# Performance work log

Measured on AMD Instinct MI355X. Metric: run time of the kernel, lower is better.

## Reference

```python
import jax, jax.numpy as jnp
import numpy as np

N_EMBD = 1024
N_HEAD = 16
HEAD_DIM = N_EMBD // N_HEAD


def setup_inputs() -> dict:
    key = jax.random.key(0)
    k1, k2, k3 = jax.random.split(key, 3)
    B, T, C = 2, 2048, N_EMBD
    x = jax.random.normal(k1, (B, T, C), dtype=jnp.float32)
    # torch nn.Linear(n_embd, 3*n_embd): weight [3C, C], bias [3C]
    W = jax.random.normal(k2, (3 * C, C), dtype=jnp.float32) * (1.0 / np.sqrt(C))
    b = jax.random.normal(k3, (3 * C,), dtype=jnp.float32) * 0.01
    return {"x": x, "W": W, "b": b}


def reference(x, W, b):
    B, T, C = x.shape
    H, D = N_HEAD, HEAD_DIM
    qkv = jnp.einsum('btc,oc->bto', x, W) + b          # [B,T,3C]
    q, k, v = jnp.split(qkv, 3, axis=2)
    # [B,H,T,D]
    q = q.reshape(B, T, H, D).transpose(0, 2, 1, 3)
    k = k.reshape(B, T, H, D).transpose(0, 2, 1, 3)
    v = v.reshape(B, T, H, D).transpose(0, 2, 1, 3)
    scale = 1.0 / np.sqrt(D).astype(np.float32)
    scores = jnp.einsum('bhid,bhjd->bhij', q, k) * scale   # [B,H,T,T]
    causal = jnp.tril(jnp.ones((T, T), dtype=bool))
    w = jnp.where(causal, jax.nn.relu(scores), 0.0)        # ReLU, no softmax
    y = jnp.einsum('bhij,bhjd->bhid', w, v)                # [B,H,T,D]
    return y.transpose(0, 2, 1, 3).reshape(B, T, C)
```

## Files before the change

### kernel.cpp

```cpp
#include <hip/hip_runtime.h>

typedef __bf16 bf16;
typedef __bf16 bf16x8 __attribute__((ext_vector_type(8)));
typedef float  f32x4  __attribute__((ext_vector_type(4)));

#define T_SEQ   2048
#define D_HEAD  64
#define NH      16
#define BH      32
#define C_EMB   1024
#define WS_STRIDE (BH * T_SEQ * D_HEAD)
#define XN (4096 * 1024)
#define WN (3072 * 1024)
#define WS_NEEDED ((size_t)(3 * WS_STRIDE + XN + WN) * 2)
#define CVT_GRID 3584

__device__ __forceinline__ bf16x8 cvt8(float4 a, float4 b) {
    bf16x8 r;
    r[0] = (__bf16)a.x; r[1] = (__bf16)a.y; r[2] = (__bf16)a.z; r[3] = (__bf16)a.w;
    r[4] = (__bf16)b.x; r[5] = (__bf16)b.y; r[6] = (__bf16)b.z; r[7] = (__bf16)b.w;
    return r;
}

__device__ __forceinline__ void gl_lds16(const bf16* g, bf16* l) {
    __builtin_amdgcn_global_load_lds(
        (const __attribute__((address_space(1))) unsigned int*)g,
        (__attribute__((address_space(3))) unsigned int*)l,
        16, 0, 0);
}

__device__ __forceinline__ unsigned pack_bf16(float a, float b) {
    union { __bf16 h[2]; unsigned u; } pk;
    pk.h[0] = (__bf16)a; pk.h[1] = (__bf16)b;
    return pk.u;
}

__global__ __launch_bounds__(256) void cvt_bf16(
    const float* __restrict__ x, const float* __restrict__ W,
    bf16* __restrict__ xb, bf16* __restrict__ wb)
{
    const int t = blockIdx.x * 256 + threadIdx.x;
    const float* src; bf16* dst; int base;
    if (t < XN / 8) { src = x; dst = xb; base = t * 8; }
    else           { src = W; dst = wb; base = (t - XN / 8) * 8; }
    float4 a = *(const float4*)(src + base);
    float4 b = *(const float4*)(src + base + 4);
    *(bf16x8*)(dst + base) = cvt8(a, b);
}

#define LDA(d, qi) {                                                          \
    const bf16* abase_ = Sh + (d)*8192 + (qi)*4096 + l15*64;                  \
    _Pragma("unroll")                                                         \
    for (int ii_ = 0; ii_ < 4; ii_++) {                                       \
        _Pragma("unroll")                                                     \
        for (int dk_ = 0; dk_ < 2; dk_++)                                     \
            aF[ii_][dk_] = *(const bf16x8*)(abase_ + ii_*1024                 \
                                            + (((dk_*4 + l4) ^ k7) * 8));     \
    }                                                                         \
}

#define LDB(d) {                                                              \
    const bf16* bbase_ = Sh + 16384 + (d)*12288 + (w*48 + l15)*64;            \
    _Pragma("unroll")                                                         \
    for (int jj_ = 0; jj_ < 3; jj_++) {                                       \
        _Pragma("unroll")                                                     \
        for (int dk_ = 0; dk_ < 2; dk_++)                                     \
            bF[jj_][dk_] = *(const bf16x8*)(bbase_ + jj_*1024                 \
                                            + (((dk_*4 + l4) ^ k7) * 8));     \
    }                                                                         \
}

#define STA(d, qi, s, ko) gl_lds16(                                           \
    aSrc + (size_t)((qi)*64 + (s)*32) * 1024 + (ko),                          \
    Sh + (d)*8192 + (qi)*4096 + (s)*2048 + w*512)

#define STB(d, u, ko) gl_lds16(                                               \
    bSrc + (size_t)((u)*32) * 1024 + (ko),                                    \
    Sh + 16384 + (d)*12288 + (u)*2048 + w*512)

#define MMA2(qi, ja, jb) {                                                    \
    __builtin_amdgcn_s_setprio(1);                                            \
    _Pragma("unroll")                                                         \
    for (int dk_ = 0; dk_ < 2; dk_++) {                                       \
        _Pragma("unroll")                                                     \
        for (int ii_ = 0; ii_ < 4; ii_++) {                                   \
            acc[(qi)*4 + ii_][ja] = __builtin_amdgcn_mfma_f32_16x16x32_bf16(  \
                aF[ii_][dk_], bF[ja][dk_], acc[(qi)*4 + ii_][ja], 0, 0, 0);   \
            acc[(qi)*4 + ii_][jb] = __builtin_amdgcn_mfma_f32_16x16x32_bf16(  \
                aF[ii_][dk_], bF[jb][dk_], acc[(qi)*4 + ii_][jb], 0, 0, 0);   \
        }                                                                     \
    }                                                                         \
    __builtin_amdgcn_s_setprio(0);                                            \
}

#define MMA1(qi, ja) {                                                        \
    __builtin_amdgcn_s_setprio(1);                                            \
    _Pragma("unroll")                                                         \
    for (int dk_ = 0; dk_ < 2; dk_++) {                                       \
        _Pragma("unroll")                                                     \
        for (int ii_ = 0; ii_ < 4; ii_++)                                     \
            acc[(qi)*4 + ii_][ja] = __builtin_amdgcn_mfma_f32_16x16x32_bf16(  \
                aF[ii_][dk_], bF[ja][dk_], acc[(qi)*4 + ii_][ja], 0, 0, 0);   \
    }                                                                         \
    __builtin_amdgcn_s_setprio(0);                                            \
}

#define BAR   __builtin_amdgcn_s_barrier()
#define LGKM0 asm volatile("s_waitcnt lgkmcnt(0)" ::: "memory")

#define HALF(d, sk)                                                           \
                                                                      \
    LDA(d, 0) LDB(d)                                                          \
    BAR; LGKM0;                                                               \
    MMA2(0, 0, 1)                                                             \
    BAR;                                                                      \
                                                \
    STB(d, 0, sk); STB(d, 1, sk); STB(d, 2, sk);                              \
    STB(d, 3, sk); STB(d, 4, sk); STB(d, 5, sk);                              \
    STA(d, 0, 0, sk); STA(d, 0, 1, sk);                                       \
    BAR;                                                                      \
    MMA1(0, 2)                                                                \
    BAR;                                                                      \
                                                                      \
    LDA(d, 1)                                                                 \
    BAR; LGKM0;                                                               \
    MMA2(1, 0, 1)                                                             \
    BAR;                                                                      \
                                                    \
    STA(d, 1, 0, sk); STA(d, 1, 1, sk);                                       \
    BAR;                                                                      \
    MMA1(1, 2)                                                                \
    asm volatile("s_waitcnt vmcnt(10)" ::: "memory");                         \
    BAR;

__global__ __launch_bounds__(256, 2) void qkv_gemm5(
    const bf16* __restrict__ xb, const bf16* __restrict__ wb,
    const float* __restrict__ bias, bf16* __restrict__ ws)
{
    __shared__ bf16 Sh[40960];

    const int tid  = threadIdx.x;
    const int lane = tid & 63;
    const int w    = tid >> 6;
    const int l15  = lane & 15, l4 = lane >> 4;
    const int k7   = l15 & 7;
    const int l8   = lane >> 3;
    const int csw  = (lane & 7) ^ l8;

    const int swz = (blockIdx.x & 7) * 64 + (blockIdx.x >> 3);
    const int bm  = swz >> 4, bn = swz & 15;

    const bf16* aSrc = xb + (size_t)(bm * 128 + w * 8 + l8) * 1024 + csw * 8;
    const bf16* bSrc = wb + (size_t)(bn * 192 + w * 8 + l8) * 1024 + csw * 8;

    f32x4 acc[8][3];
#pragma unroll
    for (int i = 0; i < 8; i++)
#pragma unroll
        for (int j = 0; j < 3; j++) acc[i][j] = (f32x4){0.f, 0.f, 0.f, 0.f};

    bf16x8 aF[4][2], bF[3][2];

    STA(0,0,0,0);  STA(0,0,1,0);  STA(0,1,0,0);  STA(0,1,1,0);
    STB(0,0,0);    STB(0,1,0);    STB(0,2,0);
    STB(0,3,0);    STB(0,4,0);    STB(0,5,0);
    STA(1,0,0,64); STA(1,0,1,64); STA(1,1,0,64); STA(1,1,1,64);
    STB(1,0,64);   STB(1,1,64);   STB(1,2,64);
    STB(1,3,64);   STB(1,4,64);   STB(1,5,64);
    asm volatile("s_waitcnt vmcnt(10)" ::: "memory");
    BAR;

    for (int it = 0; it < 8; ++it) {
        const int sk0 = (it < 7 ? (2 * it + 2) : 15) * 64;
        const int sk1 = (it < 7 ? (2 * it + 3) : 15) * 64;
        HALF(0, sk0)
        HALF(1, sk1)
    }
    asm volatile("s_waitcnt vmcnt(0)" ::: "memory");
    BAR;

    float bv[3];
#pragma unroll
    for (int ff = 0; ff < 3; ff++)
        bv[ff] = bias[bn * 192 + w * 48 + ff * 16 + l15];

    const int bi    = bm >> 4;
    const int tBase = (bm & 15) * 128;
    bf16* Wl = Sh + w * 8192;
    bf16* vt = ws + 2 * (size_t)WS_STRIDE;

#pragma unroll
    for (int ff = 0; ff < 3; ff++) {
        const int col0 = bn * 192 + w * 48 + ff * 16;
        const int wch  = col0 >> 10;
        const float qs = (wch == 0) ? 0.125f : 1.0f;
        if (wch < 2) {
#pragma unroll
            for (int i = 0; i < 8; i++)
#pragma unroll
                for (int r = 0; r < 4; r++) {
                    const int lt = i * 16 + l4 * 4 + r;
                    const int dl = l15;
                    Wl[ff * 2048 + lt * 16 + (((dl >> 3) ^ lt) & 1) * 8 + (dl & 7)]
                        = (__bf16)((acc[i][ff][r] + bv[ff]) * qs);
                }
        } else {
#pragma unroll
            for (int i = 0; i < 8; i++)
#pragma unroll
                for (int p = 0; p < 2; p++) {
                    const int lt0 = i * 16 + l4 * 4 + 2 * p;
                    const int ct  = lt0 >> 3;
                    const int dl  = l15;
                    *(unsigned*)&Wl[ff * 2048 + dl * 128
                                    + ((ct ^ dl) & 15) * 8 + (lt0 & 7)]
                        = pack_bf16(acc[i][ff][2 * p] + bv[ff],
                                    acc[i][ff][2 * p + 1] + bv[ff]);
                }
        }
    }
    __syncthreads();

#pragma unroll
    for (int ff = 0; ff < 3; ff++) {
        const int col0 = bn * 192 + w * 48 + ff * 16;
        const int wch  = col0 >> 10;
        const int cc   = col0 & 1023;
        const int hh   = cc >> 6;
        const int dd0  = cc & 63;
        if (wch < 2) {
#pragma unroll
            for (int it = 0; it < 4; it++) {
                const int lt = it * 32 + (lane >> 1);
                const int c2 = lane & 1;
                bf16x8 v8 = *(const bf16x8*)&Wl[ff * 2048 + lt * 16
                                                + ((c2 ^ lt) & 1) * 8];
                *(bf16x8*)&ws[(size_t)wch * WS_STRIDE
                              + ((size_t)(bi * NH + hh) * T_SEQ + tBase + lt) * D_HEAD
                              + dd0 + c2 * 8] = v8;
            }
        } else {
#pragma unroll
            for (int e = 0; e < 4; e++) {
                const int dl = e * 4 + l4;
                const int ct = l15;
                bf16x8 v8 = *(const bf16x8*)&Wl[ff * 2048 + dl * 128
                                                + ((ct ^ dl) & 15) * 8];
                *(bf16x8*)&vt[((size_t)(bi * NH + hh) * D_HEAD + dd0 + dl) * T_SEQ
                              + tBase + ct * 8] = v8;
            }
        }
    }
}

__global__ __launch_bounds__(256) void qkv_gemm(
    const float* __restrict__ x, const float* __restrict__ W,
    const float* __restrict__ bias, bf16* __restrict__ ws)
{
    __shared__ bf16 As[128 * 40];
    __shared__ bf16 Bs[128 * 40];

    const int tid  = threadIdx.x;
    const int lane = tid & 63;
    const int w    = tid >> 6;
    const int wm   = w >> 1, wn = w & 1;
    const int l15  = lane & 15, l4 = lane >> 4;
    const int bm   = blockIdx.x / 24, bn = blockIdx.x % 24;

    const int srow = tid >> 1;
    const int scol = (tid & 1) * 16;
    const float* xg = x + (size_t)(bm * 128 + srow) * 1024 + scol;
    const float* wg = W + (size_t)(bn * 128 + srow) * 1024 + scol;
    bf16* asw = &As[srow * 40 + scol];
    bf16* bsw = &Bs[srow * 40 + scol];

    f32x4 acc[4][4];
#pragma unroll
    for (int i = 0; i < 4; i++)
#pragma unroll
        for (int j = 0; j < 4; j++) acc[i][j] = (f32x4){0.f, 0.f, 0.f, 0.f};

    float bv[4];
#pragma unroll
    for (int j = 0; j < 4; j++) bv[j] = bias[bn * 128 + wn * 64 + j * 16 + l15];

    for (int kk = 0; kk < 32; ++kk) {
        const float* xp = xg + kk * 32;
        const float* wp = wg + kk * 32;
        float4 a0 = *(const float4*)(xp + 0);
        float4 a1 = *(const float4*)(xp + 4);
        float4 a2 = *(const float4*)(xp + 8);
        float4 a3 = *(const float4*)(xp + 12);
        float4 b0 = *(const float4*)(wp + 0);
        float4 b1 = *(const float4*)(wp + 4);
        float4 b2 = *(const float4*)(wp + 8);
        float4 b3 = *(const float4*)(wp + 12);

        __syncthreads();
        *(bf16x8*)(asw + 0) = cvt8(a0, a1);
        *(bf16x8*)(asw + 8) = cvt8(a2, a3);
        *(bf16x8*)(bsw + 0) = cvt8(b0, b1);
        *(bf16x8*)(bsw + 8) = cvt8(b2, b3);
        __syncthreads();

        bf16x8 aF[4], bF[4];
#pragma unroll
        for (int s = 0; s < 4; s++) {
            aF[s] = *(const bf16x8*)&As[(wm * 64 + s * 16 + l15) * 40 + l4 * 8];
            bF[s] = *(const bf16x8*)&Bs[(wn * 64 + s * 16 + l15) * 40 + l4 * 8];
        }
#pragma unroll
        for (int i = 0; i < 4; i++)
#pragma unroll
            for (int j = 0; j < 4; j++)
                acc[i][j] = __builtin_amdgcn_mfma_f32_16x16x32_bf16(
                    aF[i], bF[j], acc[i][j], 0, 0, 0);
    }

#pragma unroll
    for (int i = 0; i < 4; i++) {
#pragma unroll
        for (int j = 0; j < 4; j++) {
            const int n     = bn * 128 + wn * 64 + j * 16 + l15;
            const int which = n >> 10;
            const int cc    = n & 1023;
            const int h     = cc >> 6, d = cc & 63;
            const float qs  = (which == 0) ? 0.125f : 1.0f;
#pragma unroll
            for (int r = 0; r < 4; r++) {
                const int m  = bm * 128 + wm * 64 + i * 16 + l4 * 4 + r;
                const int bi = m >> 11, t = m & 2047;
                const int bh = bi * NH + h;
                const float v = (acc[i][j][r] + bv[j]) * qs;
                size_t idx;
                if (which == 2)
                    idx = 2 * (size_t)WS_STRIDE + ((size_t)bh * D_HEAD + d) * T_SEQ + t;
                else
                    idx = (size_t)which * WS_STRIDE + ((size_t)bh * T_SEQ + t) * D_HEAD + d;
                ws[idx] = (__bf16)v;
            }
        }
    }
}

#define KSTAGE(jt_, p_) {                                                     \
    _Pragma("unroll")                                                         \
    for (int e_ = 0; e_ < 4; e_++) {                                          \
        const int rb_ = w * 32 + e_ * 8;                                      \
        gl_lds16(kg + (size_t)((jt_) * 128 + rb_ + ksub) * 64                 \
                    + ((kc ^ ksub ^ (e_ << 1)) * 8),                          \
                 &Kb[p_][rb_ * 64]);                                          \
    }                                                                         \
}

#define VSTAGE(jt_) {                                                         \
    _Pragma("unroll")                                                         \
    for (int e_ = 0; e_ < 4; e_++) {                                          \
        const int rb_ = w * 16 + e_ * 4;                                      \
        const int sw_ = (rb_ & 12) + vsub;                 \
        gl_lds16(vt + (size_t)(rb_ + vsub) * T_SEQ + (jt_) * 128              \
                    + ((vc ^ sw_) * 8),                                       \
                 &Vts[rb_ * 128]);                                            \
    }                                                                         \
}

__global__ __launch_bounds__(256) void attn(
    const bf16* __restrict__ ws, float* __restrict__ out)
{
    __shared__ bf16 Kb[2][128 * 64];
    __shared__ bf16 Vts[64 * 128];

    const int tid  = threadIdx.x;
    const int lane = tid & 63;
    const int w    = tid >> 6;
    const int l15  = lane & 15, qd = lane >> 4;

    const int bh = blockIdx.x & 31;
    const int u  = blockIdx.x >> 5;
    const int s  = 31 - u;
    const int qt = s >> 1;
    const int hs = s & 1;
    const int nj = qt + 1;
    const int qb = s * 64;

    const bf16* qg = ws + (size_t)bh * (T_SEQ * D_HEAD);
    const bf16* kg = ws + WS_STRIDE + (size_t)bh * (T_SEQ * D_HEAD);
    const bf16* vt = ws + 2 * (size_t)WS_STRIDE + (size_t)bh * (D_HEAD * T_SEQ);
    const int b = bh >> 4, h = bh & 15;

    const int ksub = lane >> 3;
    const int kc   = lane & 7;
    const int vsub = qd;
    const int vc   = l15;

    const int krow0 = 8 * (l15 >> 2) + (l15 & 3);
    const int pos00 = qd ^ (l15 & 3) ^ ((l15 >> 2) << 1);
    const int kbO0  = krow0 * 64 + pos00 * 8;
    const int kbO1  = krow0 * 64 + (pos00 ^ 4) * 8;

    bf16x8 qF[2];
#pragma unroll
    for (int dk = 0; dk < 2; dk++)
        qF[dk] = *(const bf16x8*)(qg
            + (qb + w * 16 + l15) * 64 + dk * 32 + qd * 8);

    f32x4 o[4];
#pragma unroll
    for (int sd = 0; sd < 4; sd++) o[sd] = (f32x4){0.f, 0.f, 0.f, 0.f};

    KSTAGE(0, 0);

    for (int jt = 0; jt < nj; ++jt) {
        const int p = jt & 1;
        const bool more = (jt + 1 < nj);
        VSTAGE(jt);
        if (more) {
            KSTAGE(jt + 1, p ^ 1);
            asm volatile("s_waitcnt vmcnt(8)" ::: "memory");
        } else {
            asm volatile("s_waitcnt vmcnt(4)" ::: "memory");
        }
        BAR;

        const bf16* kb0 = &Kb[p][kbO0];
        const bf16* kb1 = &Kb[p][kbO1];

        const bool need_mask = (jt == nj - 1);
        const int mMax = (need_mask && hs == 0) ? 2 : 4;
        unsigned PK[8][2];
#pragma unroll
        for (int m = 0; m < 4; m++) {
            if (m < mMax) {
                bf16x8 kf[2][2];
                kf[0][0] = *(const bf16x8*)(kb0 + m * 2048);
                kf[0][1] = *(const bf16x8*)(kb1 + m * 2048);
                kf[1][0] = *(const bf16x8*)(kb1 + m * 2048 + 256);
                kf[1][1] = *(const bf16x8*)(kb0 + m * 2048 + 256);
#pragma unroll
                for (int h2 = 0; h2 < 2; h2++) {
                    const int kn = 2 * m + h2;
                    f32x4 s0 = {0.f, 0.f, 0.f, 0.f};
                    __builtin_amdgcn_s_setprio(1);
                    s0 = __builtin_amdgcn_mfma_f32_16x16x32_bf16(kf[h2][0], qF[0], s0, 0, 0, 0);
                    s0 = __builtin_amdgcn_mfma_f32_16x16x32_bf16(kf[h2][1], qF[1], s0, 0, 0, 0);
                    __builtin_amdgcn_s_setprio(0);
                    const int keyb = jt * 128 + 32 * m + 8 * qd + 4 * h2;
                    float v[4];
#pragma unroll
                    for (int r = 0; r < 4; r++) v[r] = fmaxf(s0[r], 0.f);
                    if (need_mask) {
                        const int q = qb + w * 16 + l15;
#pragma unroll
                        for (int r = 0; r < 4; r++)
                            if (q < keyb + r) v[r] = 0.f;
                    }
                    PK[kn][0] = pack_bf16(v[0], v[1]);
                    PK[kn][1] = pack_bf16(v[2], v[3]);
                }
            }
        }

        if (more) asm volatile("s_waitcnt vmcnt(4)" ::: "memory");
        else      asm volatile("s_waitcnt vmcnt(0)" ::: "memory");
        BAR;

#pragma unroll
        for (int kk = 0; kk < 4; kk++) {
            if (kk < mMax) {
                union { unsigned dw[4]; bf16x8 v; } uu;
                uu.dw[0] = PK[2 * kk + 0][0];
                uu.dw[1] = PK[2 * kk + 0][1];
                uu.dw[2] = PK[2 * kk + 1][0];
                uu.dw[3] = PK[2 * kk + 1][1];
                const bf16x8 pF = uu.v;
                __builtin_amdgcn_s_setprio(1);
#pragma unroll
                for (int sd = 0; sd < 4; sd++) {
                    bf16x8 vf = *(const bf16x8*)&Vts[(sd * 16 + l15) * 128
                                                     + (((kk * 4 + qd) ^ l15) * 8)];
                    o[sd] = __builtin_amdgcn_mfma_f32_16x16x32_bf16(pF, vf, o[sd], 0, 0, 0);
                }
                __builtin_amdgcn_s_setprio(0);
            }
        }

        BAR;
    }

#pragma unroll
    for (int sd = 0; sd < 4; sd++) {
        const int d = sd * 16 + l15;
#pragma unroll
        for (int r = 0; r < 4; r++) {
            const int t = qb + w * 16 + qd * 4 + r;
            out[((size_t)b * T_SEQ + t) * C_EMB + h * 64 + d] = o[sd][r];
        }
    }
}

extern "C" void kernel_launch(void* const* d_in, const int* in_sizes, int n_in,
                              void* d_out, int out_size, void* d_ws, size_t ws_size,
                              hipStream_t stream) {
    const float* x    = (const float*)d_in[0];
    const float* W    = (const float*)d_in[1];
    const float* bias = (const float*)d_in[2];
    float* out        = (float*)d_out;
    bf16*  ws         = (bf16*)d_ws;

    if (ws_size >= WS_NEEDED) {
        bf16* xb = ws + 3 * (size_t)WS_STRIDE;
        bf16* wb = xb + XN;
        cvt_bf16<<<dim3(CVT_GRID), dim3(256), 0, stream>>>(x, W, xb, wb);
        qkv_gemm5<<<dim3(512), dim3(256), 0, stream>>>(xb, wb, bias, ws);
    } else {
        qkv_gemm<<<dim3(768), dim3(256), 0, stream>>>(x, W, bias, ws);
    }
    attn<<<dim3(1024), dim3(256), 0, stream>>>(ws, out);
}
```

Measured before the change: 138.3 us.

## Shrink attention key tiles to 64 and double-buffer V alongside K

Reduces the key/value tile from 128 to 64 keys per iteration and double-buffers both K and V in shared memory, so V for the next tile is prefetched together with K. This drops the mid-iteration wait and barrier between the QK and PV phases and removes the half-tile masking logic. Shared memory per block falls from 48KB to 32KB and launch bounds now request 4 blocks per SM to raise occupancy. The cost is twice as many loop iterations and barriers per query tile, plus register pressure from the occupancy hint.

```diff
diff --git a/kernel.cpp b/kernel.cpp
--- a/kernel.cpp
+++ b/kernel.cpp
@@ -345,30 +345,29 @@
 
 #define KSTAGE(jt_, p_) {                                                     \
     _Pragma("unroll")                                                         \
-    for (int e_ = 0; e_ < 4; e_++) {                                          \
-        const int rb_ = w * 32 + e_ * 8;                                      \
-        gl_lds16(kg + (size_t)((jt_) * 128 + rb_ + ksub) * 64                 \
-                    + ((kc ^ ksub ^ (e_ << 1)) * 8),                          \
+    for (int e_ = 0; e_ < 2; e_++) {                                          \
+        const int rb_ = w * 16 + e_ * 8;                                      \
+        gl_lds16(kg + (size_t)((jt_) * 64 + rb_ + ksub) * 64                  \
+                    + ((kc ^ ksub ^ (((w * 2 + e_) & 3) << 1)) * 8),          \
                  &Kb[p_][rb_ * 64]);                                          \
     }                                                                         \
 }
 
-#define VSTAGE(jt_) {                                                         \
+#define VSTAGE(jt_, p_) {                                                     \
     _Pragma("unroll")                                                         \
-    for (int e_ = 0; e_ < 4; e_++) {                                          \
-        const int rb_ = w * 16 + e_ * 4;                                      \
-        const int sw_ = (rb_ & 12) + vsub;                 \
-        gl_lds16(vt + (size_t)(rb_ + vsub) * T_SEQ + (jt_) * 128              \
-                    + ((vc ^ sw_) * 8),                                       \
-                 &Vts[rb_ * 128]);                                            \
+    for (int e_ = 0; e_ < 2; e_++) {                                          \
+        const int rb_ = w * 16 + e_ * 8;                                      \
+        gl_lds16(vt + (size_t)(rb_ + ksub) * T_SEQ + (jt_) * 64               \
+                    + ((kc ^ ksub) * 8),                                      \
+                 &Vb[p_][rb_ * 64]);                                          \
     }                                                                         \
 }
 
-__global__ __launch_bounds__(256) void attn(
+__global__ __launch_bounds__(256, 4) void attn(
     const bf16* __restrict__ ws, float* __restrict__ out)
 {
-    __shared__ bf16 Kb[2][128 * 64];
-    __shared__ bf16 Vts[64 * 128];
+    __shared__ bf16 Kb[2][64 * 64];
+    __shared__ bf16 Vb[2][64 * 64];
 
     const int tid  = threadIdx.x;
     const int lane = tid & 63;
@@ -378,9 +377,7 @@
     const int bh = blockIdx.x & 31;
     const int u  = blockIdx.x >> 5;
     const int s  = 31 - u;
-    const int qt = s >> 1;
-    const int hs = s & 1;
-    const int nj = qt + 1;
+    const int nj = s + 1;
     const int qb = s * 64;
 
     const bf16* qg = ws + (size_t)bh * (T_SEQ * D_HEAD);
@@ -390,8 +387,6 @@
 
     const int ksub = lane >> 3;
     const int kc   = lane & 7;
-    const int vsub = qd;
-    const int vc   = l15;
 
     const int krow0 = 8 * (l15 >> 2) + (l15 & 3);
     const int pos00 = qd ^ (l15 & 3) ^ ((l15 >> 2) << 1);
@@ -409,16 +404,16 @@
     for (int sd = 0; sd < 4; sd++) o[sd] = (f32x4){0.f, 0.f, 0.f, 0.f};
 
     KSTAGE(0, 0);
+    VSTAGE(0, 0);
 
     for (int jt = 0; jt < nj; ++jt) {
         const int p = jt & 1;
-        const bool more = (jt + 1 < nj);
-        VSTAGE(jt);
-        if (more) {
+        if (jt + 1 < nj) {
             KSTAGE(jt + 1, p ^ 1);
-            asm volatile("s_waitcnt vmcnt(8)" ::: "memory");
+            VSTAGE(jt + 1, p ^ 1);
+            asm volatile("s_waitcnt vmcnt(4)" ::: "memory");
         } else {
-            asm volatile("s_waitcnt vmcnt(4)" ::: "memory");
+            asm volatile("s_waitcnt vmcnt(0)" ::: "memory");
         }
         BAR;
 
@@ -426,62 +421,53 @@
         const bf16* kb1 = &Kb[p][kbO1];
 
         const bool need_mask = (jt == nj - 1);
-        const int mMax = (need_mask && hs == 0) ? 2 : 4;
-        unsigned PK[8][2];
-#pragma unroll
-        for (int m = 0; m < 4; m++) {
-            if (m < mMax) {
-                bf16x8 kf[2][2];
-                kf[0][0] = *(const bf16x8*)(kb0 + m * 2048);
-                kf[0][1] = *(const bf16x8*)(kb1 + m * 2048);
-                kf[1][0] = *(const bf16x8*)(kb1 + m * 2048 + 256);
-                kf[1][1] = *(const bf16x8*)(kb0 + m * 2048 + 256);
-#pragma unroll
-                for (int h2 = 0; h2 < 2; h2++) {
-                    const int kn = 2 * m + h2;
-                    f32x4 s0 = {0.f, 0.f, 0.f, 0.f};
-                    __builtin_amdgcn_s_setprio(1);
-                    s0 = __builtin_amdgcn_mfma_f32_16x16x32_bf16(kf[h2][0], qF[0], s0, 0, 0, 0);
-                    s0 = __builtin_amdgcn_mfma_f32_16x16x32_bf16(kf[h2][1], qF[1], s0, 0, 0, 0);
-                    __builtin_amdgcn_s_setprio(0);
-                    const int keyb = jt * 128 + 32 * m + 8 * qd + 4 * h2;
-                    float v[4];
-#pragma unroll
-                    for (int r = 0; r < 4; r++) v[r] = fmaxf(s0[r], 0.f);
-                    if (need_mask) {
-                        const int q = qb + w * 16 + l15;
-#pragma unroll
-                        for (int r = 0; r < 4; r++)
-                            if (q < keyb + r) v[r] = 0.f;
-                    }
-                    PK[kn][0] = pack_bf16(v[0], v[1]);
-                    PK[kn][1] = pack_bf16(v[2], v[3]);
+        unsigned PK[4][2];
+#pragma unroll
+        for (int m = 0; m < 2; m++) {
+            bf16x8 kf[2][2];
+            kf[0][0] = *(const bf16x8*)(kb0 + m * 2048);
+            kf[0][1] = *(const bf16x8*)(kb1 + m * 2048);
+            kf[1][0] = *(const bf16x8*)(kb1 + m * 2048 + 256);
+            kf[1][1] = *(const bf16x8*)(kb0 + m * 2048 + 256);
+#pragma unroll
+            for (int h2 = 0; h2 < 2; h2++) {
+                const int kn = 2 * m + h2;
+                f32x4 s0 = {0.f, 0.f, 0.f, 0.f};
+                __builtin_amdgcn_s_setprio(1);
+                s0 = __builtin_amdgcn_mfma_f32_16x16x32_bf16(kf[h2][0], qF[0], s0, 0, 0, 0);
+                s0 = __builtin_amdgcn_mfma_f32_16x16x32_bf16(kf[h2][1], qF[1], s0, 0, 0, 0);
+                __builtin_amdgcn_s_setprio(0);
+                const int keyb = jt * 64 + 32 * m + 8 * qd + 4 * h2;
+                float v[4];
+#pragma unroll
+                for (int r = 0; r < 4; r++) v[r] = fmaxf(s0[r], 0.f);
+                if (need_mask) {
+                    const int q = qb + w * 16 + l15;
+#pragma unroll
+                    for (int r = 0; r < 4; r++)
+                        if (q < keyb + r) v[r] = 0.f;
                 }
+                PK[kn][0] = pack_bf16(v[0], v[1]);
+                PK[kn][1] = pack_bf16(v[2], v[3]);
             }
         }
 
-        if (more) asm volatile("s_waitcnt vmcnt(4)" ::: "memory");
-        else      asm volatile("s_waitcnt vmcnt(0)" ::: "memory");
-        BAR;
-
-#pragma unroll
-        for (int kk = 0; kk < 4; kk++) {
-            if (kk < mMax) {
-                union { unsigned dw[4]; bf16x8 v; } uu;
-                uu.dw[0] = PK[2 * kk + 0][0];
-                uu.dw[1] = PK[2 * kk + 0][1];
-                uu.dw[2] = PK[2 * kk + 1][0];
-                uu.dw[3] = PK[2 * kk + 1][1];
-                const bf16x8 pF = uu.v;
-                __builtin_amdgcn_s_setprio(1);
-#pragma unroll
-                for (int sd = 0; sd < 4; sd++) {
-                    bf16x8 vf = *(const bf16x8*)&Vts[(sd * 16 + l15) * 128
-                                                     + (((kk * 4 + qd) ^ l15) * 8)];
-                    o[sd] = __builtin_amdgcn_mfma_f32_16x16x32_bf16(pF, vf, o[sd], 0, 0, 0);
-                }
-                __builtin_amdgcn_s_setprio(0);
+#pragma unroll
+        for (int kk = 0; kk < 2; kk++) {
+            union { unsigned dw[4]; bf16x8 v; } uu;
+            uu.dw[0] = PK[2 * kk + 0][0];
+            uu.dw[1] = PK[2 * kk + 0][1];
+            uu.dw[2] = PK[2 * kk + 1][0];
+            uu.dw[3] = PK[2 * kk + 1][1];
+            const bf16x8 pF = uu.v;
+            __builtin_amdgcn_s_setprio(1);
+#pragma unroll
+            for (int sd = 0; sd < 4; sd++) {
+                bf16x8 vf = *(const bf16x8*)&Vb[p][(sd * 16 + l15) * 64
+                                                   + (((kk * 4 + qd) ^ (l15 & 7)) * 8)];
+                o[sd] = __builtin_amdgcn_mfma_f32_16x16x32_bf16(pF, vf, o[sd], 0, 0, 0);
             }
+            __builtin_amdgcn_s_setprio(0);
         }
 
         BAR;
```

New measurement: 142.1 us. 2.7% more time.

## Load all A/B fragments up front and collapse half-step barriers in QKV GEMM

Applied to the files above, without the earlier changes.

Each half-iteration of the QKV GEMM now reads both A sub-tiles and the B tile from LDS into registers at once. It then issues all global-to-LDS prefetches and runs all MFMAs in one block, going from six barriers per half to two. The goal is to cut barrier and synchronisation overhead and give longer uninterrupted MFMA runs. The cost is more vector registers for the second A fragment set, which could affect occupancy at launch bounds 256,2, and less interleaving of loads with MFMAs.

```diff
diff --git a/kernel.cpp b/kernel.cpp
--- a/kernel.cpp
+++ b/kernel.cpp
@@ -48,13 +48,13 @@
     *(bf16x8*)(dst + base) = cvt8(a, b);
 }
 
-#define LDA(d, qi) {                                                          \
+#define LDAq(d, qi, dst) {                                                    \
     const bf16* abase_ = Sh + (d)*8192 + (qi)*4096 + l15*64;                  \
     _Pragma("unroll")                                                         \
     for (int ii_ = 0; ii_ < 4; ii_++) {                                       \
         _Pragma("unroll")                                                     \
         for (int dk_ = 0; dk_ < 2; dk_++)                                     \
-            aF[ii_][dk_] = *(const bf16x8*)(abase_ + ii_*1024                 \
+            dst[ii_][dk_] = *(const bf16x8*)(abase_ + ii_*1024                \
                                             + (((dk_*4 + l4) ^ k7) * 8));     \
     }                                                                         \
 }
@@ -78,62 +78,40 @@
     bSrc + (size_t)((u)*32) * 1024 + (ko),                                    \
     Sh + 16384 + (d)*12288 + (u)*2048 + w*512)
 
-#define MMA2(qi, ja, jb) {                                                    \
-    __builtin_amdgcn_s_setprio(1);                                            \
+#define MMAQ(qi, src) {                                                       \
     _Pragma("unroll")                                                         \
     for (int dk_ = 0; dk_ < 2; dk_++) {                                       \
         _Pragma("unroll")                                                     \
         for (int ii_ = 0; ii_ < 4; ii_++) {                                   \
-            acc[(qi)*4 + ii_][ja] = __builtin_amdgcn_mfma_f32_16x16x32_bf16(  \
-                aF[ii_][dk_], bF[ja][dk_], acc[(qi)*4 + ii_][ja], 0, 0, 0);   \
-            acc[(qi)*4 + ii_][jb] = __builtin_amdgcn_mfma_f32_16x16x32_bf16(  \
-                aF[ii_][dk_], bF[jb][dk_], acc[(qi)*4 + ii_][jb], 0, 0, 0);   \
+            _Pragma("unroll")                                                 \
+            for (int jj_ = 0; jj_ < 3; jj_++)                                 \
+                acc[(qi)*4 + ii_][jj_] =                                      \
+                    __builtin_amdgcn_mfma_f32_16x16x32_bf16(                  \
+                        src[ii_][dk_], bF[jj_][dk_],                          \
+                        acc[(qi)*4 + ii_][jj_], 0, 0, 0);                     \
         }                                                                     \
     }                                                                         \
-    __builtin_amdgcn_s_setprio(0);                                            \
-}
-
-#define MMA1(qi, ja) {                                                        \
-    __builtin_amdgcn_s_setprio(1);                                            \
-    _Pragma("unroll")                                                         \
-    for (int dk_ = 0; dk_ < 2; dk_++) {                                       \
-        _Pragma("unroll")                                                     \
-        for (int ii_ = 0; ii_ < 4; ii_++)                                     \
-            acc[(qi)*4 + ii_][ja] = __builtin_amdgcn_mfma_f32_16x16x32_bf16(  \
-                aF[ii_][dk_], bF[ja][dk_], acc[(qi)*4 + ii_][ja], 0, 0, 0);   \
-    }                                                                         \
-    __builtin_amdgcn_s_setprio(0);                                            \
 }
 
 #define BAR   __builtin_amdgcn_s_barrier()
 #define LGKM0 asm volatile("s_waitcnt lgkmcnt(0)" ::: "memory")
 
 #define HALF(d, sk)                                                           \
-                                                                      \
-    LDA(d, 0) LDB(d)                                                          \
-    BAR; LGKM0;                                                               \
-    MMA2(0, 0, 1)                                                             \
-    BAR;                                                                      \
-                                                \
+    LDAq(d, 0, aF0) LDAq(d, 1, aF1) LDB(d)                                    \
+    LGKM0;                                                                    \
+    BAR;         \
     STB(d, 0, sk); STB(d, 1, sk); STB(d, 2, sk);                              \
     STB(d, 3, sk); STB(d, 4, sk); STB(d, 5, sk);                              \
     STA(d, 0, 0, sk); STA(d, 0, 1, sk);                                       \
-    BAR;                                                                      \
-    MMA1(0, 2)                                                                \
-    BAR;                                                                      \
-                                                                      \
-    LDA(d, 1)                                                                 \
-    BAR; LGKM0;                                                               \
-    MMA2(1, 0, 1)                                                             \
-    BAR;                                                                      \
-                                                    \
     STA(d, 1, 0, sk); STA(d, 1, 1, sk);                                       \
-    BAR;                                                                      \
-    MMA1(1, 2)                                                                \
-    asm volatile("s_waitcnt vmcnt(10)" ::: "memory");                         \
+    __builtin_amdgcn_s_setprio(1);                                            \
+    MMAQ(0, aF0)                                                              \
+    MMAQ(1, aF1)                                                              \
+    __builtin_amdgcn_s_setprio(0);                                            \
+    asm volatile("s_waitcnt vmcnt(10)" ::: "memory");    \
     BAR;
 
-__global__ __launch_bounds__(256, 2) void qkv_gemm5(
+__global__ __launch_bounds__(256, 2) void qkv_gemm6(
     const bf16* __restrict__ xb, const bf16* __restrict__ wb,
     const float* __restrict__ bias, bf16* __restrict__ ws)
 {
@@ -159,7 +137,7 @@
 #pragma unroll
         for (int j = 0; j < 3; j++) acc[i][j] = (f32x4){0.f, 0.f, 0.f, 0.f};
 
-    bf16x8 aF[4][2], bF[3][2];
+    bf16x8 aF0[4][2], aF1[4][2], bF[3][2];
 
     STA(0,0,0,0);  STA(0,0,1,0);  STA(0,1,0,0);  STA(0,1,1,0);
     STB(0,0,0);    STB(0,1,0);    STB(0,2,0);
@@ -511,7 +489,7 @@
         bf16* xb = ws + 3 * (size_t)WS_STRIDE;
         bf16* wb = xb + XN;
         cvt_bf16<<<dim3(CVT_GRID), dim3(256), 0, stream>>>(x, W, xb, wb);
-        qkv_gemm5<<<dim3(512), dim3(256), 0, stream>>>(xb, wb, bias, ws);
+        qkv_gemm6<<<dim3(512), dim3(256), 0, stream>>>(xb, wb, bias, ws);
     } else {
         qkv_gemm<<<dim3(768), dim3(256), 0, stream>>>(x, W, bias, ws);
     }
```

Result: no change. 136.2 us (-1.6%).
